# Performance work log

Hardware: AMD Instinct MI355X
Metric: run time of the kernel (lower is better)

## Reference

```python
import jax, jax.numpy as jnp
import numpy as np

MARGIN = 0.2


def setup_inputs() -> dict:
    key = jax.random.key(0)
    k1, k2 = jax.random.split(key)
    B, D = 384, 256
    x = jax.random.normal(k1, (B, D), dtype=jnp.float32)
    labels = jax.random.randint(k2, (B,), 0, 32, dtype=jnp.int32)
    return {"x": x, "labels": labels}


def reference(x, labels):
    # Batch-all triplet loss, faithful to the torch loop:
    #  - anchor/positive pairs are combinations (a < p) within a class
    #  - negatives are all samples of a different class
    #  - the torch loop iterates over every label OCCURRENCE, so each class's
    #    triplet set is appended k_c times (k_c = class size); this is a
    #    per-triplet weight of k_{label[a]} in the mean.
    B = x.shape[0]
    # pairwise squared distances, computed as elementwise diff^2 sum (matches torch math)
    diff = x[:, None, :] - x[None, :, :]          # [B,B,D]
    dist2 = jnp.sum(diff * diff, axis=-1)         # [B,B]

    same = labels[:, None] == labels[None, :]     # [B,B]
    idx = jnp.arange(B)
    ap_mask = same & (idx[:, None] < idx[None, :])  # anchor<positive, same class
    neg_mask = ~same                               # negatives: different class

    # class size for each sample = duplication factor from the python loop
    counts = jnp.sum(same.astype(jnp.float32), axis=1)  # [B]

    valid = ap_mask[:, :, None] & neg_mask[:, None, :]  # [B,B,B]
    w = valid.astype(jnp.float32) * counts[:, None, None]

    # loss[a,p,n] = relu(margin + d(a,p) - d(a,n))
    losses = jax.nn.relu(MARGIN + dist2[:, :, None] - dist2[:, None, :])

    num = jnp.sum(w * losses)
    den = jnp.sum(w)
    return jnp.where(den > 0, num / den, jnp.float32(0.0))
```

## Files before the change

### kernel.cpp

```cpp
#include <hip/hip_runtime.h>

#define BB 384
#define DD 256
#define F4 (DD / 4)
#define APB 2
#define NBLK (BB / APB)
#define MARGIN 0.2f

__global__ __launch_bounds__(256) void triplet_fused_kernel(
    const float* __restrict__ x,
    const int* __restrict__ labels,
    double* __restrict__ partial_num,
    double* __restrict__ partial_den) {
    __shared__ int    s_lab[BB];
    __shared__ float  s_d[APB][BB];
    __shared__ int    s_pos[BB];
    __shared__ int    s_np, s_cnt;
    __shared__ double s_red[4];

    const int tid  = threadIdx.x;
    const int wave = tid >> 6;
    const int lane = tid & 63;
    const int rr   = lane >> 4;
    const int dd   = lane & 15;
    const int a0   = blockIdx.x * APB;

    const float4* x4 = reinterpret_cast<const float4*>(x);

    for (int i = tid; i < BB; i += 256) s_lab[i] = labels[i];

    float4 xa[APB][4];
#pragma unroll
    for (int j = 0; j < APB; ++j)
#pragma unroll
        for (int k = 0; k < 4; ++k)
            xa[j][k] = x4[(a0 + j) * F4 + k * 16 + dd];

    for (int b0 = wave * 96; b0 < wave * 96 + 96; b0 += 4) {
        const int b = b0 + rr;
        float4 row[4];
#pragma unroll
        for (int k = 0; k < 4; ++k)
            row[k] = x4[b * F4 + k * 16 + dd];

        float s[APB];
#pragma unroll
        for (int j = 0; j < APB; ++j) {
            float sx = 0.f, sy = 0.f, sz = 0.f, sw = 0.f;
#pragma unroll
            for (int k = 0; k < 4; ++k) {
                float dx = row[k].x - xa[j][k].x;
                float dy = row[k].y - xa[j][k].y;
                float dz = row[k].z - xa[j][k].z;
                float dw = row[k].w - xa[j][k].w;
                sx += dx * dx;
                sy += dy * dy;
                sz += dz * dz;
                sw += dw * dw;
            }
            s[j] = (sx + sy) + (sz + sw);
        }
#pragma unroll
        for (int mask = 1; mask < 16; mask <<= 1)
#pragma unroll
            for (int j = 0; j < APB; ++j)
                s[j] += __shfl_xor(s[j], mask, 64);

        if (dd == 0) s_d[0][b] = s[0];
        if (dd == 1) s_d[1][b] = s[1];
    }
    __syncthreads();

    for (int j = 0; j < APB; ++j) {
        const int a = a0 + j;
        if (tid == 0) { s_np = 0; s_cnt = 0; }
        __syncthreads();

        const int la = s_lab[a];
        for (int i = tid; i < BB; i += 256) {
            if (s_lab[i] == la) {
                atomicAdd(&s_cnt, 1);
                if (i > a) {
                    int k = atomicAdd(&s_np, 1);
                    s_pos[k] = i;
                }
            }
        }
        __syncthreads();

        const int np = s_np;
        const int cnt = s_cnt;

        double num_local = 0.0;
        for (int pi = 0; pi < np; ++pi) {
            const float t = MARGIN + s_d[j][s_pos[pi]];
            for (int n = tid; n < BB; n += 256) {
                if (s_lab[n] != la) {
                    float l = t - s_d[j][n];
                    if (l > 0.f) num_local += (double)l;
                }
            }
        }

        for (int off = 32; off > 0; off >>= 1)
            num_local += __shfl_down(num_local, off, 64);
        if (lane == 0) s_red[wave] = num_local;
        __syncthreads();

        if (tid == 0) {
            double tot = (s_red[0] + s_red[1]) + (s_red[2] + s_red[3]);
            partial_num[a] = tot * (double)cnt;
            partial_den[a] = (double)cnt * (double)np * (double)(BB - cnt);
        }
        __syncthreads();
    }
}

__global__ __launch_bounds__(256) void finalize_kernel(
    const double* __restrict__ partial_num,
    const double* __restrict__ partial_den,
    float* __restrict__ out) {
    __shared__ double s_red[8];
    const int tid = threadIdx.x;

    double n_local = 0.0, d_local = 0.0;
    for (int i = tid; i < BB; i += 256) {
        n_local += partial_num[i];
        d_local += partial_den[i];
    }
    for (int off = 32; off > 0; off >>= 1) {
        n_local += __shfl_down(n_local, off, 64);
        d_local += __shfl_down(d_local, off, 64);
    }
    const int lane = tid & 63, wid = tid >> 6;
    if (lane == 0) { s_red[wid] = n_local; s_red[4 + wid] = d_local; }
    __syncthreads();

    if (tid == 0) {
        double num = (s_red[0] + s_red[1]) + (s_red[2] + s_red[3]);
        double den = (s_red[4] + s_red[5]) + (s_red[6] + s_red[7]);
        out[0] = (den > 0.0) ? (float)(num / den) : 0.0f;
    }
}

extern "C" void kernel_launch(void* const* d_in, const int* in_sizes, int n_in,
                              void* d_out, int out_size, void* d_ws, size_t ws_size,
                              hipStream_t stream) {
    const float* x = (const float*)d_in[0];
    const int* labels = (const int*)d_in[1];
    float* out = (float*)d_out;

    double* partial_num = (double*)d_ws;
    double* partial_den = partial_num + BB;

    triplet_fused_kernel<<<NBLK, 256, 0, stream>>>(x, labels, partial_num, partial_den);
    finalize_kernel<<<1, 256, 0, stream>>>(partial_num, partial_den, out);
}
```

Baseline: 80.29 us.

## Process both anchors concurrently with 512 threads and swap triplet loop order

Doubles the block to 512 threads so each half handles one anchor at once, replacing the sequential per-anchor loop and several barriers. The distance phase is split across 8 waves. Positive thresholds (margin + d_ap) are precomputed into shared memory, and the loop is inverted so each thread keeps its negative distance in a register while sweeping the positives. The cost is a larger block, which may lower occupancy, while the per-anchor serialization and repeated shared loads go away.

```diff
diff --git a/kernel.cpp b/kernel.cpp
--- a/kernel.cpp
+++ b/kernel.cpp
@@ -5,18 +5,19 @@
 #define F4 (DD / 4)
 #define APB 2
 #define NBLK (BB / APB)
+#define NT 512
 #define MARGIN 0.2f
 
-__global__ __launch_bounds__(256) void triplet_fused_kernel(
+__global__ __launch_bounds__(NT) void triplet_fused_kernel(
     const float* __restrict__ x,
     const int* __restrict__ labels,
     double* __restrict__ partial_num,
     double* __restrict__ partial_den) {
     __shared__ int    s_lab[BB];
     __shared__ float  s_d[APB][BB];
-    __shared__ int    s_pos[BB];
-    __shared__ int    s_np, s_cnt;
-    __shared__ double s_red[4];
+    __shared__ float  s_t[APB][BB];
+    __shared__ int    s_np[APB], s_cnt[APB];
+    __shared__ double s_red[8];
 
     const int tid  = threadIdx.x;
     const int wave = tid >> 6;
@@ -27,7 +28,7 @@
 
     const float4* x4 = reinterpret_cast<const float4*>(x);
 
-    for (int i = tid; i < BB; i += 256) s_lab[i] = labels[i];
+    for (int i = tid; i < BB; i += NT) s_lab[i] = labels[i];
 
     float4 xa[APB][4];
 #pragma unroll
@@ -36,7 +37,9 @@
         for (int k = 0; k < 4; ++k)
             xa[j][k] = x4[(a0 + j) * F4 + k * 16 + dd];
 
-    for (int b0 = wave * 96; b0 < wave * 96 + 96; b0 += 4) {
+    const int rbeg = wave * 48;
+#pragma unroll 2
+    for (int b0 = rbeg; b0 < rbeg + 48; b0 += 4) {
         const int b = b0 + rr;
         float4 row[4];
 #pragma unroll
@@ -69,50 +72,54 @@
         if (dd == 0) s_d[0][b] = s[0];
         if (dd == 1) s_d[1][b] = s[1];
     }
+
+    const int half = tid >> 8;
+    const int t2   = tid & 255;
+    const int a    = a0 + half;
+
+    if (t2 == 0) { s_np[half] = 0; s_cnt[half] = 0; }
     __syncthreads();
 
-    for (int j = 0; j < APB; ++j) {
-        const int a = a0 + j;
-        if (tid == 0) { s_np = 0; s_cnt = 0; }
-        __syncthreads();
-
-        const int la = s_lab[a];
-        for (int i = tid; i < BB; i += 256) {
-            if (s_lab[i] == la) {
-                atomicAdd(&s_cnt, 1);
-                if (i > a) {
-                    int k = atomicAdd(&s_np, 1);
-                    s_pos[k] = i;
-                }
+    const int la = s_lab[a];
+    const float* dj = s_d[half];
+    for (int i = t2; i < BB; i += 256) {
+        if (s_lab[i] == la) {
+            atomicAdd(&s_cnt[half], 1);
+            if (i > a) {
+                int k = atomicAdd(&s_np[half], 1);
+                s_t[half][k] = MARGIN + dj[i];
             }
         }
-        __syncthreads();
+    }
+    __syncthreads();
 
-        const int np = s_np;
-        const int cnt = s_cnt;
+    const int np  = s_np[half];
+    const int cnt = s_cnt[half];
 
-        double num_local = 0.0;
-        for (int pi = 0; pi < np; ++pi) {
-            const float t = MARGIN + s_d[j][s_pos[pi]];
-            for (int n = tid; n < BB; n += 256) {
-                if (s_lab[n] != la) {
-                    float l = t - s_d[j][n];
-                    if (l > 0.f) num_local += (double)l;
-                }
+    double num_local = 0.0;
+    for (int n = t2; n < BB; n += 256) {
+        if (s_lab[n] != la) {
+            const float dn = dj[n];
+            for (int pi = 0; pi < np; ++pi) {
+                float l = s_t[half][pi] - dn;
+                if (l > 0.f) num_local += (double)l;
             }
         }
+    }
 
-        for (int off = 32; off > 0; off >>= 1)
-            num_local += __shfl_down(num_local, off, 64);
-        if (lane == 0) s_red[wave] = num_local;
-        __syncthreads();
+    for (int off = 32; off > 0; off >>= 1)
+        num_local += __shfl_down(num_local, off, 64);
+    if (lane == 0) s_red[wave] = num_local;
+    __syncthreads();
 
-        if (tid == 0) {
-            double tot = (s_red[0] + s_red[1]) + (s_red[2] + s_red[3]);
-            partial_num[a] = tot * (double)cnt;
-            partial_den[a] = (double)cnt * (double)np * (double)(BB - cnt);
-        }
-        __syncthreads();
+    if (tid == 0) {
+        double tot = (s_red[0] + s_red[1]) + (s_red[2] + s_red[3]);
+        partial_num[a] = tot * (double)cnt;
+        partial_den[a] = (double)cnt * (double)np * (double)(BB - cnt);
+    } else if (tid == 256) {
+        double tot = (s_red[4] + s_red[5]) + (s_red[6] + s_red[7]);
+        partial_num[a] = tot * (double)cnt;
+        partial_den[a] = (double)cnt * (double)np * (double)(BB - cnt);
     }
 }
 
@@ -153,6 +160,6 @@
     double* partial_num = (double*)d_ws;
     double* partial_den = partial_num + BB;
 
-    triplet_fused_kernel<<<NBLK, 256, 0, stream>>>(x, labels, partial_num, partial_den);
+    triplet_fused_kernel<<<NBLK, NT, 0, stream>>>(x, labels, partial_num, partial_den);
     finalize_kernel<<<1, 256, 0, stream>>>(partial_num, partial_den, out);
 }
```

Result: faster. 65.54 us (-18.4%).
